# Kernel tuning notes

Hardware: AMD Instinct MI355X
Metric: run time of the kernel (lower is better)

The kernel has to match this reference:

```python
import jax, jax.numpy as jnp
import numpy as np

B, LI, LJ, D = 32, 512, 512, 512
NN_DIM = 256  # agg output dim = 2*NN_DIM = 512


def setup_inputs() -> dict:
    key = jax.random.key(0)
    k1, k2, k3 = jax.random.split(key, 3)
    i = jax.random.normal(k1, (B, LI, D), dtype=jnp.float32)
    j = jax.random.normal(k2, (B, LJ, D), dtype=jnp.float32)
    W_agg = jax.random.normal(k3, (D, 2 * NN_DIM), dtype=jnp.float32) * (1.0 / np.sqrt(D))
    b_agg = jnp.zeros((2 * NN_DIM,), dtype=jnp.float32)
    return {"i": i, "j": j, "W_agg": W_agg, "b_agg": b_agg}


def _agg(x, W, b):
    # shared aggregation net: Dense(2*nn_dim) + tanh, then mean-pool over time
    # x: [B, L, D] -> [B, 2*nn_dim]
    return jnp.mean(jnp.tanh(jnp.einsum('bld,dh->blh', x, W) + b), axis=1)


def reference(i, j, W_agg, b_agg):
    # cross-attention scores: [B, Li, Lj]
    weight = jnp.einsum('bik,bjk->bij', i, j)
    # row softmax (over Lj) -> weights to aggregate j per i-position
    weight_j = jax.nn.softmax(weight, axis=2)
    # column softmax (over Li) -> weights to aggregate i per j-position
    weight_i = jax.nn.softmax(weight, axis=1)
    weighted_i = jnp.einsum('bij,bid->bjd', weight_i, i)  # [B, Lj, D]
    weighted_j = jnp.einsum('bij,bjd->bid', weight_j, j)  # [B, Li, D]
    output_i = jnp.abs(i - weighted_j)  # [B, Li, D]
    output_j = jnp.abs(j - weighted_i)  # [B, Lj, D]
    oi = _agg(output_i, W_agg, b_agg)   # [B, 2*nn_dim]
    oj = _agg(output_j, W_agg, b_agg)   # [B, 2*nn_dim]
    # K.mean(K.stack([oi, oj], axis=1), axis=1)
    return 0.5 * (oi + oj)
```

## Files before the change

### kernel.cpp

```cpp
#include <hip/hip_runtime.h>
#include <math.h>

#define B_ 32
#define L_ 512
#define D_ 512
#define H_ 512

typedef unsigned short u16;
typedef _Float16 h16;
typedef h16 half8 __attribute__((ext_vector_type(8)));
typedef float f32x4 __attribute__((ext_vector_type(4)));

#define SW(r, c) ((c) ^ (((r) >> 1) & 3))

typedef __attribute__((address_space(1))) void gvoid;
typedef __attribute__((address_space(3))) void svoid;
__device__ __forceinline__ void async_cp16(const void* g, void* l) {
    __builtin_amdgcn_global_load_lds((gvoid*)g, (svoid*)l, 16, 0, 0);
}

__device__ __forceinline__ u16 f2h(float x) {
    h16 h = (h16)x;
    u16 r;
    __builtin_memcpy(&r, &h, 2);
    return r;
}
__device__ __forceinline__ float h2f(u16 u) {
    h16 h;
    __builtin_memcpy(&h, &u, 2);
    return (float)h;
}
__device__ __forceinline__ float fast_tanh(float x) {
    return 1.0f - 2.0f / (__expf(2.0f * x) + 1.0f);
}

__device__ __forceinline__ void xcd_decode16(int n, int& z, int& tile) {
    int xcd = n & 7, w = n >> 3;
    z = xcd + 8 * (w >> 4);
    tile = w & 15;
}

__global__ __launch_bounds__(256) void cvt_all(const float* __restrict__ I,
                                               const float* __restrict__ Jm,
                                               const float* __restrict__ W,
                                               u16* __restrict__ Ih, u16* __restrict__ IhT,
                                               u16* __restrict__ Jh, u16* __restrict__ JhT,
                                               u16* __restrict__ WT,
                                               float* __restrict__ out) {
    const int z = blockIdx.z;
    const float* src;
    u16* h;
    u16* hT;
    size_t base;
    if (z < 32) {
        src = I; h = Ih; hT = IhT; base = (size_t)z * 512 * 512;
    } else if (z < 64) {
        src = Jm; h = Jh; hT = JhT; base = (size_t)(z - 32) * 512 * 512;
    } else {
        src = W; h = nullptr; hT = WT; base = 0;
        out[(blockIdx.y * 8 + blockIdx.x) * 256 + threadIdx.x] = 0.0f;
    }
    const int r0 = blockIdx.y * 64, c0 = blockIdx.x * 64;
    __shared__ u16 t[64][66];
    const int tid = threadIdx.x;
    const int tr = tid >> 4, tc4 = (tid & 15) * 4;
#pragma unroll
    for (int rep = 0; rep < 4; ++rep) {
        int r = rep * 16 + tr;
        f32x4 v = *(const f32x4*)(src + base + (size_t)(r0 + r) * 512 + c0 + tc4);
        unsigned h0 = f2h(v[0]), h1 = f2h(v[1]), h2 = f2h(v[2]), h3 = f2h(v[3]);
        if (h)
            *(uint2*)(h + base + (size_t)(r0 + r) * 512 + c0 + tc4) =
                make_uint2(h0 | (h1 << 16), h2 | (h3 << 16));
        t[r][tc4] = (u16)h0; t[r][tc4 + 1] = (u16)h1;
        t[r][tc4 + 2] = (u16)h2; t[r][tc4 + 3] = (u16)h3;
    }
    __syncthreads();
#pragma unroll
    for (int rep = 0; rep < 4; ++rep) {
        int r = rep * 16 + tr;
        unsigned a = t[tc4][r], b = t[tc4 + 1][r], c = t[tc4 + 2][r], d = t[tc4 + 3][r];
        *(uint2*)(hT + base + (size_t)(c0 + r) * 512 + r0 + tc4) =
            make_uint2(a | (b << 16), c | (d << 16));
    }
}

__global__ __launch_bounds__(256, 2) void score_mfma(const u16* __restrict__ Ih,
                                                     const u16* __restrict__ Jh,
                                                     u16* __restrict__ P_un,
                                                     u16* __restrict__ P_unT,
                                                     float* __restrict__ rtmax,
                                                     float* __restrict__ rtsum,
                                                     float* __restrict__ ctmax,
                                                     float* __restrict__ ctsum) {
    int b, tile;
    xcd_decode16(blockIdx.x, b, tile);
    const int i0 = (tile >> 2) * 128, j0 = (tile & 3) * 128;
    __shared__ u16 Ah[128 * 32], Bh[128 * 32];
    const int tid = threadIdx.x;
    const int wave = tid >> 6, lane = tid & 63;
    const int wm = (wave >> 1) * 64, wn = (wave & 1) * 64;
    const int lr = lane & 15, q = lane >> 4;
    const size_t boff = (size_t)b * L_ * D_;
    const u16* Ibh = Ih + boff;
    const u16* Jbh = Jh + boff;

    f32x4 acc[4][4] = {};

    for (int k0 = 0; k0 < D_; k0 += 32) {
#pragma unroll
        for (int h = 0; h < 2; ++h) {
            int g = wave * 2 + h;
            int r = g * 16 + (lane >> 2);
            int cg = SW(r, lane & 3);
            async_cp16(Ibh + (size_t)(i0 + r) * D_ + k0 + cg * 8, (char*)Ah + g * 1024);
            async_cp16(Jbh + (size_t)(j0 + r) * D_ + k0 + cg * 8, (char*)Bh + g * 1024);
        }
        __syncthreads();
        half8 af[4], bf[4];
#pragma unroll
        for (int mi = 0; mi < 4; ++mi) {
            int r = wm + mi * 16 + lr;
            af[mi] = *(const half8*)&Ah[r * 32 + SW(r, q) * 8];
        }
#pragma unroll
        for (int ni = 0; ni < 4; ++ni) {
            int r = wn + ni * 16 + lr;
            bf[ni] = *(const half8*)&Bh[r * 32 + SW(r, q) * 8];
        }
#pragma unroll
        for (int mi = 0; mi < 4; ++mi)
#pragma unroll
            for (int ni = 0; ni < 4; ++ni)
                acc[mi][ni] = __builtin_amdgcn_mfma_f32_16x16x32_f16(af[mi], bf[ni], acc[mi][ni], 0, 0, 0);
        __syncthreads();
    }

    float rm[4][4];
#pragma unroll
    for (int mi = 0; mi < 4; ++mi)
#pragma unroll
        for (int r4 = 0; r4 < 4; ++r4) {
            float t = fmaxf(fmaxf(acc[mi][0][r4], acc[mi][1][r4]),
                            fmaxf(acc[mi][2][r4], acc[mi][3][r4]));
#pragma unroll
            for (int off = 1; off < 16; off <<= 1) t = fmaxf(t, __shfl_xor(t, off));
            rm[mi][r4] = t;
        }
    float cm[4];
#pragma unroll
    for (int ni = 0; ni < 4; ++ni) {
        float u = -1e30f;
#pragma unroll
        for (int mi = 0; mi < 4; ++mi)
#pragma unroll
            for (int r4 = 0; r4 < 4; ++r4) u = fmaxf(u, acc[mi][ni][r4]);
        u = fmaxf(u, __shfl_xor(u, 16));
        u = fmaxf(u, __shfl_xor(u, 32));
        cm[ni] = u;
    }

    u16* Pu_b = P_un + (size_t)b * L_ * L_;
    u16* PuT_b = P_unT + (size_t)b * L_ * L_;
    float rs[4][4] = {};
    float cs[4] = {};
#pragma unroll
    for (int mi = 0; mi < 4; ++mi)
#pragma unroll
        for (int ni = 0; ni < 4; ++ni) {
            int i_base = i0 + wm + mi * 16 + q * 4;
            int j = j0 + wn + ni * 16 + lr;
            unsigned pc[4];
#pragma unroll
            for (int r4 = 0; r4 < 4; ++r4) {
                float er = __expf(acc[mi][ni][r4] - rm[mi][r4]);
                rs[mi][r4] += er;
                Pu_b[(size_t)(i_base + r4) * L_ + j] = f2h(er);
                float ec = __expf(acc[mi][ni][r4] - cm[ni]);
                cs[ni] += ec;
                pc[r4] = f2h(ec);
            }
            *(uint2*)&PuT_b[(size_t)j * L_ + i_base] =
                make_uint2(pc[0] | (pc[1] << 16), pc[2] | (pc[3] << 16));
        }

    const int gr = (j0 + wn) >> 6;
    const int gc = (i0 + wm) >> 6;
#pragma unroll
    for (int mi = 0; mi < 4; ++mi)
#pragma unroll
        for (int r4 = 0; r4 < 4; ++r4) {
            float s = rs[mi][r4];
#pragma unroll
            for (int off = 1; off < 16; off <<= 1) s += __shfl_xor(s, off);
            if (lr == 0) {
                int i = i0 + wm + mi * 16 + q * 4 + r4;
                rtmax[((size_t)b * L_ + i) * 8 + gr] = rm[mi][r4];
                rtsum[((size_t)b * L_ + i) * 8 + gr] = s;
            }
        }
#pragma unroll
    for (int ni = 0; ni < 4; ++ni) {
        float s = cs[ni];
        s += __shfl_xor(s, 16);
        s += __shfl_xor(s, 32);
        if (q == 0) {
            int j = j0 + wn + ni * 16 + lr;
            ctmax[((size_t)b * L_ + j) * 8 + gc] = cm[ni];
            ctsum[((size_t)b * L_ + j) * 8 + gc] = s;
        }
    }
}

__global__ __launch_bounds__(256, 2) void absdiff_scaled(const u16* __restrict__ P_un,
                                                         const u16* __restrict__ P_unT,
                                                         const float* __restrict__ rtmax,
                                                         const float* __restrict__ rtsum,
                                                         const float* __restrict__ ctmax,
                                                         const float* __restrict__ ctsum,
                                                         const u16* __restrict__ JhT,
                                                         const u16* __restrict__ IhT,
                                                         const u16* __restrict__ Ih,
                                                         const u16* __restrict__ Jh,
                                                         u16* __restrict__ Xall) {
    int zz, tile;
    xcd_decode16(blockIdx.x, zz, tile);
    const int side = zz >> 5, b = zz & 31;
    const int a0 = (tile >> 2) * 128, d0 = (tile & 3) * 128;
    const u16* Pb = (side ? P_unT : P_un) + (size_t)b * L_ * L_;
    const float* tmax = (side ? ctmax : rtmax) + (size_t)b * L_ * 8;
    const float* tsum = (side ? ctsum : rtsum) + (size_t)b * L_ * 8;
    const u16* Vt = (side ? IhT : JhT) + (size_t)b * D_ * L_;
    const u16* Oh = (side ? Jh : Ih) + (size_t)b * L_ * D_;
    u16* Xb = Xall + (size_t)zz * L_ * D_;

    __shared__ u16 As[128 * 32], Bs[128 * 32];
    __shared__ float sc[8][128];
    const int tid = threadIdx.x;
    const int wave = tid >> 6, lane = tid & 63;
    const int wm = (wave >> 1) * 64, wn = (wave & 1) * 64;
    const int lr = lane & 15, q = lane >> 4;

    if (tid < 128) {
        const float* tm = tmax + (size_t)(a0 + tid) * 8;
        const float* ts = tsum + (size_t)(a0 + tid) * 8;
        f32x4 m0 = *(const f32x4*)tm, m1 = *(const f32x4*)(tm + 4);
        f32x4 s0 = *(const f32x4*)ts, s1 = *(const f32x4*)(ts + 4);
        float m = fmaxf(fmaxf(fmaxf(m0[0], m0[1]), fmaxf(m0[2], m0[3])),
                        fmaxf(fmaxf(m1[0], m1[1]), fmaxf(m1[2], m1[3])));
        float e0 = __expf(m0[0] - m), e1 = __expf(m0[1] - m);
        float e2 = __expf(m0[2] - m), e3 = __expf(m0[3] - m);
        float e4 = __expf(m1[0] - m), e5 = __expf(m1[1] - m);
        float e6 = __expf(m1[2] - m), e7 = __expf(m1[3] - m);
        float inv = 1.0f / (e0 * s0[0] + e1 * s0[1] + e2 * s0[2] + e3 * s0[3] +
                            e4 * s1[0] + e5 * s1[1] + e6 * s1[2] + e7 * s1[3]);
        sc[0][tid] = e0 * inv; sc[1][tid] = e1 * inv;
        sc[2][tid] = e2 * inv; sc[3][tid] = e3 * inv;
        sc[4][tid] = e4 * inv; sc[5][tid] = e5 * inv;
        sc[6][tid] = e6 * inv; sc[7][tid] = e7 * inv;
    }
    __syncthreads();

    f32x4 acc[4][4] = {};

    for (int k0 = 0; k0 < L_; k0 += 32) {
#pragma unroll
        for (int h = 0; h < 2; ++h) {
            int g = wave * 2 + h;
            int r = g * 16 + (lane >> 2);
            int cg = SW(r, lane & 3);
            async_cp16(Pb + (size_t)(a0 + r) * L_ + k0 + cg * 8, (char*)As + g * 1024);
            async_cp16(Vt + (size_t)(d0 + r) * L_ + k0 + cg * 8, (char*)Bs + g * 1024);
        }
        __syncthreads();
        const int gk = k0 >> 6;
        half8 af[4], bf[4];
#pragma unroll
        for (int mi = 0; mi < 4; ++mi) {
            int r = wm + mi * 16 + lr;
            h16 s = (h16)sc[gk][r];
            half8 s8 = {s, s, s, s, s, s, s, s};
            af[mi] = *(const half8*)&As[r * 32 + SW(r, q) * 8] * s8;
        }
#pragma unroll
        for (int ni = 0; ni < 4; ++ni) {
            int r = wn + ni * 16 + lr;
            bf[ni] = *(const half8*)&Bs[r * 32 + SW(r, q) * 8];
        }
#pragma unroll
        for (int mi = 0; mi < 4; ++mi)
#pragma unroll
            for (int ni = 0; ni < 4; ++ni)
                acc[mi][ni] = __builtin_amdgcn_mfma_f32_16x16x32_f16(af[mi], bf[ni], acc[mi][ni], 0, 0, 0);
        __syncthreads();
    }

#pragma unroll
    for (int mi = 0; mi < 4; ++mi)
#pragma unroll
        for (int ni = 0; ni < 4; ++ni) {
            int i = a0 + wm + mi * 16 + q * 4;
            int d = d0 + wn + ni * 16 + lr;
#pragma unroll
            for (int r4 = 0; r4 < 4; ++r4) {
                float x = fabsf(h2f(Oh[(size_t)(i + r4) * D_ + d]) - acc[mi][ni][r4]);
                Xb[(size_t)(i + r4) * D_ + d] = f2h(x);
            }
        }
}

__global__ __launch_bounds__(256, 2) void agg_mfma(const u16* __restrict__ Xall,
                                                   const u16* __restrict__ Wt,
                                                   const float* __restrict__ bias,
                                                   float* __restrict__ out) {
    int zz, tile;
    xcd_decode16(blockIdx.x, zz, tile);
    const int bb = zz & 31;
    const u16* Xb = Xall + (size_t)zz * L_ * D_;
    const int l0 = (tile >> 2) * 128, h0 = (tile & 3) * 128;
    __shared__ u16 As[128 * 32], Bs[128 * 32];
    const int tid = threadIdx.x;
    const int wave = tid >> 6, lane = tid & 63;
    const int wm = (wave >> 1) * 64, wn = (wave & 1) * 64;
    const int lr = lane & 15, q = lane >> 4;

    f32x4 acc[4][4] = {};

    for (int k0 = 0; k0 < D_; k0 += 32) {
#pragma unroll
        for (int h = 0; h < 2; ++h) {
            int g = wave * 2 + h;
            int r = g * 16 + (lane >> 2);
            int cg = SW(r, lane & 3);
            async_cp16(Xb + (size_t)(l0 + r) * D_ + k0 + cg * 8, (char*)As + g * 1024);
            async_cp16(Wt + (size_t)(h0 + r) * D_ + k0 + cg * 8, (char*)Bs + g * 1024);
        }
        __syncthreads();
        half8 af[4], bf[4];
#pragma unroll
        for (int mi = 0; mi < 4; ++mi) {
            int r = wm + mi * 16 + lr;
            af[mi] = *(const half8*)&As[r * 32 + SW(r, q) * 8];
        }
#pragma unroll
        for (int ni = 0; ni < 4; ++ni) {
            int r = wn + ni * 16 + lr;
            bf[ni] = *(const half8*)&Bs[r * 32 + SW(r, q) * 8];
        }
#pragma unroll
        for (int mi = 0; mi < 4; ++mi)
#pragma unroll
            for (int ni = 0; ni < 4; ++ni)
                acc[mi][ni] = __builtin_amdgcn_mfma_f32_16x16x32_f16(af[mi], bf[ni], acc[mi][ni], 0, 0, 0);
        __syncthreads();
    }

#pragma unroll
    for (int ni = 0; ni < 4; ++ni) {
        int hcol = h0 + wn + ni * 16 + lr;
        float bsv = bias[hcol];
        float ssum = 0.f;
#pragma unroll
        for (int mi = 0; mi < 4; ++mi)
#pragma unroll
            for (int r4 = 0; r4 < 4; ++r4)
                ssum += fast_tanh(acc[mi][ni][r4] + bsv);
        ssum += __shfl_xor(ssum, 16);
        ssum += __shfl_xor(ssum, 32);
        if (q == 0) atomicAdd(&out[bb * H_ + hcol], ssum * (0.5f / (float)L_));
    }
}

extern "C" void kernel_launch(void* const* d_in, const int* in_sizes, int n_in,
                              void* d_out, int out_size, void* d_ws, size_t ws_size,
                              hipStream_t stream) {
    const float* I = (const float*)d_in[0];
    const float* Jm = (const float*)d_in[1];
    const float* W = (const float*)d_in[2];
    const float* bias = (const float*)d_in[3];
    float* out = (float*)d_out;

    const size_t BLD = (size_t)B_ * L_ * D_;
    const size_t BLL = (size_t)B_ * L_ * L_;

    char* p = (char*)d_ws;
    auto give = [&](size_t bytes) {
        char* r = p;
        p += (bytes + 255) & ~(size_t)255;
        return r;
    };
    u16* Ih = (u16*)give(BLD * 2);
    u16* Jh = (u16*)give(BLD * 2);
    u16* IhT = (u16*)give(BLD * 2);
    u16* JhT = (u16*)give(BLD * 2);
    u16* WT = (u16*)give((size_t)D_ * H_ * 2);
    u16* P_un = (u16*)give(BLL * 2);
    u16* P_unT = (u16*)give(BLL * 2);
    float* rtmax = (float*)give((size_t)B_ * L_ * 8 * 4);
    float* rtsum = (float*)give((size_t)B_ * L_ * 8 * 4);
    float* ctmax = (float*)give((size_t)B_ * L_ * 8 * 4);
    float* ctsum = (float*)give((size_t)B_ * L_ * 8 * 4);
    u16* Xall = (u16*)give(2 * BLD * 2);

    cvt_all<<<dim3(8, 8, 65), 256, 0, stream>>>(I, Jm, W, Ih, IhT, Jh, JhT, WT, out);
    score_mfma<<<512, 256, 0, stream>>>(Ih, Jh, P_un, P_unT, rtmax, rtsum, ctmax, ctsum);
    absdiff_scaled<<<1024, 256, 0, stream>>>(P_un, P_unT, rtmax, rtsum, ctmax, ctsum,
                                             JhT, IhT, Ih, Jh, Xall);
    agg_mfma<<<1024, 256, 0, stream>>>(Xall, WT, bias, out);
}
```

Before: 190.3 us.

## Fuse absdiff and aggregation GEMMs into one kernel keeping X in LDS

Merges the weighted-sum/abs-diff kernel and the Dense+tanh+mean aggregation kernel into one kernel. Each block handles a 64-row slab over the full D, keeps the fp16 abs-diff tile in shared memory, then multiplies it by W directly. This removes the 32 MB Xall round trip through global memory and one launch. In exchange the grid drops to 512 blocks with 64-row tiles, so there is less reuse per MFMA tile. Shared memory per block grows to about 75 KB, which can lower occupancy.

```diff
diff --git a/kernel.cpp b/kernel.cpp
--- a/kernel.cpp
+++ b/kernel.cpp
@@ -38,6 +38,11 @@
     int xcd = n & 7, w = n >> 3;
     z = xcd + 8 * (w >> 4);
     tile = w & 15;
+}
+__device__ __forceinline__ void xcd_decode8(int n, int& z, int& tile) {
+    int xcd = n & 7, w = n >> 3;
+    z = xcd + 8 * (w >> 3);
+    tile = w & 7;
 }
 
 __global__ __launch_bounds__(256) void cvt_all(const float* __restrict__ I,
@@ -212,38 +217,41 @@
     }
 }
 
-__global__ __launch_bounds__(256, 2) void absdiff_scaled(const u16* __restrict__ P_un,
-                                                         const u16* __restrict__ P_unT,
-                                                         const float* __restrict__ rtmax,
-                                                         const float* __restrict__ rtsum,
-                                                         const float* __restrict__ ctmax,
-                                                         const float* __restrict__ ctsum,
-                                                         const u16* __restrict__ JhT,
-                                                         const u16* __restrict__ IhT,
-                                                         const u16* __restrict__ Ih,
-                                                         const u16* __restrict__ Jh,
-                                                         u16* __restrict__ Xall) {
-    int zz, tile;
-    xcd_decode16(blockIdx.x, zz, tile);
+__global__ __launch_bounds__(256, 2) void fused_tail(const u16* __restrict__ P_un,
+                                                     const u16* __restrict__ P_unT,
+                                                     const float* __restrict__ rtmax,
+                                                     const float* __restrict__ rtsum,
+                                                     const float* __restrict__ ctmax,
+                                                     const float* __restrict__ ctsum,
+                                                     const u16* __restrict__ JhT,
+                                                     const u16* __restrict__ IhT,
+                                                     const u16* __restrict__ Ih,
+                                                     const u16* __restrict__ Jh,
+                                                     const u16* __restrict__ Wt,
+                                                     const float* __restrict__ bias,
+                                                     float* __restrict__ out) {
+    int zz, ltile;
+    xcd_decode8(blockIdx.x, zz, ltile);
     const int side = zz >> 5, b = zz & 31;
-    const int a0 = (tile >> 2) * 128, d0 = (tile & 3) * 128;
+    const int l0 = ltile * 64;
     const u16* Pb = (side ? P_unT : P_un) + (size_t)b * L_ * L_;
     const float* tmax = (side ? ctmax : rtmax) + (size_t)b * L_ * 8;
     const float* tsum = (side ? ctsum : rtsum) + (size_t)b * L_ * 8;
     const u16* Vt = (side ? IhT : JhT) + (size_t)b * D_ * L_;
     const u16* Oh = (side ? Jh : Ih) + (size_t)b * L_ * D_;
-    u16* Xb = Xall + (size_t)zz * L_ * D_;
-
-    __shared__ u16 As[128 * 32], Bs[128 * 32];
-    __shared__ float sc[8][128];
+
+    __shared__ u16 Xs[64][520];
+    __shared__ u16 As[64 * 32];
+    __shared__ u16 Bs[128 * 32];
+    __shared__ float sc[8][64];
     const int tid = threadIdx.x;
     const int wave = tid >> 6, lane = tid & 63;
-    const int wm = (wave >> 1) * 64, wn = (wave & 1) * 64;
+    const int wm = (wave >> 1) * 32, wn = (wave & 1) * 64;
     const int lr = lane & 15, q = lane >> 4;
 
-    if (tid < 128) {
-        const float* tm = tmax + (size_t)(a0 + tid) * 8;
-        const float* ts = tsum + (size_t)(a0 + tid) * 8;
+    if (tid < 64) {
+        const float* tm = tmax + (size_t)(l0 + tid) * 8;
+        const float* ts = tsum + (size_t)(l0 + tid) * 8;
         f32x4 m0 = *(const f32x4*)tm, m1 = *(const f32x4*)(tm + 4);
         f32x4 s0 = *(const f32x4*)ts, s1 = *(const f32x4*)(ts + 4);
         float m = fmaxf(fmaxf(fmaxf(m0[0], m0[1]), fmaxf(m0[2], m0[3])),
@@ -261,113 +269,107 @@
     }
     __syncthreads();
 
-    f32x4 acc[4][4] = {};
-
-    for (int k0 = 0; k0 < L_; k0 += 32) {
-#pragma unroll
-        for (int h = 0; h < 2; ++h) {
-            int g = wave * 2 + h;
-            int r = g * 16 + (lane >> 2);
-            int cg = SW(r, lane & 3);
-            async_cp16(Pb + (size_t)(a0 + r) * L_ + k0 + cg * 8, (char*)As + g * 1024);
-            async_cp16(Vt + (size_t)(d0 + r) * L_ + k0 + cg * 8, (char*)Bs + g * 1024);
-        }
-        __syncthreads();
-        const int gk = k0 >> 6;
-        half8 af[4], bf[4];
-#pragma unroll
-        for (int mi = 0; mi < 4; ++mi) {
-            int r = wm + mi * 16 + lr;
-            h16 s = (h16)sc[gk][r];
-            half8 s8 = {s, s, s, s, s, s, s, s};
-            af[mi] = *(const half8*)&As[r * 32 + SW(r, q) * 8] * s8;
+#pragma unroll 1
+    for (int c = 0; c < 4; ++c) {
+        const int d0 = c * 128;
+        f32x4 acc[2][4] = {};
+        for (int k0 = 0; k0 < L_; k0 += 32) {
+            {
+                int r = wave * 16 + (lane >> 2);
+                int cg = SW(r, lane & 3);
+                async_cp16(Pb + (size_t)(l0 + r) * L_ + k0 + cg * 8, (char*)As + wave * 1024);
+            }
+#pragma unroll
+            for (int h = 0; h < 2; ++h) {
+                int g = wave * 2 + h;
+                int r = g * 16 + (lane >> 2);
+                int cg = SW(r, lane & 3);
+                async_cp16(Vt + (size_t)(d0 + r) * L_ + k0 + cg * 8, (char*)Bs + g * 1024);
+            }
+            __syncthreads();
+            const int gk = k0 >> 6;
+            half8 af[2], bf[4];
+#pragma unroll
+            for (int mi = 0; mi < 2; ++mi) {
+                int r = wm + mi * 16 + lr;
+                h16 s = (h16)sc[gk][r];
+                half8 s8 = {s, s, s, s, s, s, s, s};
+                af[mi] = *(const half8*)&As[r * 32 + SW(r, q) * 8] * s8;
+            }
+#pragma unroll
+            for (int ni = 0; ni < 4; ++ni) {
+                int r = wn + ni * 16 + lr;
+                bf[ni] = *(const half8*)&Bs[r * 32 + SW(r, q) * 8];
+            }
+#pragma unroll
+            for (int mi = 0; mi < 2; ++mi)
+#pragma unroll
+                for (int ni = 0; ni < 4; ++ni)
+                    acc[mi][ni] = __builtin_amdgcn_mfma_f32_16x16x32_f16(af[mi], bf[ni], acc[mi][ni], 0, 0, 0);
+            __syncthreads();
+        }
+#pragma unroll
+        for (int mi = 0; mi < 2; ++mi)
+#pragma unroll
+            for (int ni = 0; ni < 4; ++ni) {
+                int row = wm + mi * 16 + q * 4;
+                int col = wn + ni * 16 + lr;
+#pragma unroll
+                for (int r4 = 0; r4 < 4; ++r4) {
+                    float x = fabsf(h2f(Oh[(size_t)(l0 + row + r4) * D_ + d0 + col]) -
+                                    acc[mi][ni][r4]);
+                    Xs[row + r4][d0 + col] = f2h(x);
+                }
+            }
+    }
+    __syncthreads();
+
+    const int bb = b;
+#pragma unroll 1
+    for (int c = 0; c < 4; ++c) {
+        const int h0 = c * 128;
+        f32x4 acc[2][4] = {};
+        for (int k0 = 0; k0 < D_; k0 += 32) {
+#pragma unroll
+            for (int h = 0; h < 2; ++h) {
+                int g = wave * 2 + h;
+                int r = g * 16 + (lane >> 2);
+                int cg = SW(r, lane & 3);
+                async_cp16(Wt + (size_t)(h0 + r) * D_ + k0 + cg * 8, (char*)Bs + g * 1024);
+            }
+            __syncthreads();
+            half8 af[2], bf[4];
+#pragma unroll
+            for (int mi = 0; mi < 2; ++mi) {
+                int r = wm + mi * 16 + lr;
+                af[mi] = *(const half8*)&Xs[r][k0 + q * 8];
+            }
+#pragma unroll
+            for (int ni = 0; ni < 4; ++ni) {
+                int r = wn + ni * 16 + lr;
+                bf[ni] = *(const half8*)&Bs[r * 32 + SW(r, q) * 8];
+            }
+#pragma unroll
+            for (int mi = 0; mi < 2; ++mi)
+#pragma unroll
+                for (int ni = 0; ni < 4; ++ni)
+                    acc[mi][ni] = __builtin_amdgcn_mfma_f32_16x16x32_f16(af[mi], bf[ni], acc[mi][ni], 0, 0, 0);
+            __syncthreads();
         }
 #pragma unroll
         for (int ni = 0; ni < 4; ++ni) {
-            int r = wn + ni * 16 + lr;
-            bf[ni] = *(const half8*)&Bs[r * 32 + SW(r, q) * 8];
-        }
-#pragma unroll
-        for (int mi = 0; mi < 4; ++mi)
-#pragma unroll
-            for (int ni = 0; ni < 4; ++ni)
-                acc[mi][ni] = __builtin_amdgcn_mfma_f32_16x16x32_f16(af[mi], bf[ni], acc[mi][ni], 0, 0, 0);
-        __syncthreads();
-    }
-
-#pragma unroll
-    for (int mi = 0; mi < 4; ++mi)
-#pragma unroll
-        for (int ni = 0; ni < 4; ++ni) {
-            int i = a0 + wm + mi * 16 + q * 4;
-            int d = d0 + wn + ni * 16 + lr;
-#pragma unroll
-            for (int r4 = 0; r4 < 4; ++r4) {
-                float x = fabsf(h2f(Oh[(size_t)(i + r4) * D_ + d]) - acc[mi][ni][r4]);
-                Xb[(size_t)(i + r4) * D_ + d] = f2h(x);
-            }
-        }
-}
-
-__global__ __launch_bounds__(256, 2) void agg_mfma(const u16* __restrict__ Xall,
-                                                   const u16* __restrict__ Wt,
-                                                   const float* __restrict__ bias,
-                                                   float* __restrict__ out) {
-    int zz, tile;
-    xcd_decode16(blockIdx.x, zz, tile);
-    const int bb = zz & 31;
-    const u16* Xb = Xall + (size_t)zz * L_ * D_;
-    const int l0 = (tile >> 2) * 128, h0 = (tile & 3) * 128;
-    __shared__ u16 As[128 * 32], Bs[128 * 32];
-    const int tid = threadIdx.x;
-    const int wave = tid >> 6, lane = tid & 63;
-    const int wm = (wave >> 1) * 64, wn = (wave & 1) * 64;
-    const int lr = lane & 15, q = lane >> 4;
-
-    f32x4 acc[4][4] = {};
-
-    for (int k0 = 0; k0 < D_; k0 += 32) {
-#pragma unroll
-        for (int h = 0; h < 2; ++h) {
-            int g = wave * 2 + h;
-            int r = g * 16 + (lane >> 2);
-            int cg = SW(r, lane & 3);
-            async_cp16(Xb + (size_t)(l0 + r) * D_ + k0 + cg * 8, (char*)As + g * 1024);
-            async_cp16(Wt + (size_t)(h0 + r) * D_ + k0 + cg * 8, (char*)Bs + g * 1024);
-        }
-        __syncthreads();
-        half8 af[4], bf[4];
-#pragma unroll
-        for (int mi = 0; mi < 4; ++mi) {
-            int r = wm + mi * 16 + lr;
-            af[mi] = *(const half8*)&As[r * 32 + SW(r, q) * 8];
-        }
-#pragma unroll
-        for (int ni = 0; ni < 4; ++ni) {
-            int r = wn + ni * 16 + lr;
-            bf[ni] = *(const half8*)&Bs[r * 32 + SW(r, q) * 8];
-        }
-#pragma unroll
-        for (int mi = 0; mi < 4; ++mi)
-#pragma unroll
-            for (int ni = 0; ni < 4; ++ni)
-                acc[mi][ni] = __builtin_amdgcn_mfma_f32_16x16x32_f16(af[mi], bf[ni], acc[mi][ni], 0, 0, 0);
-        __syncthreads();
-    }
-
-#pragma unroll
-    for (int ni = 0; ni < 4; ++ni) {
-        int hcol = h0 + wn + ni * 16 + lr;
-        float bsv = bias[hcol];
-        float ssum = 0.f;
-#pragma unroll
-        for (int mi = 0; mi < 4; ++mi)
-#pragma unroll
-            for (int r4 = 0; r4 < 4; ++r4)
-                ssum += fast_tanh(acc[mi][ni][r4] + bsv);
-        ssum += __shfl_xor(ssum, 16);
-        ssum += __shfl_xor(ssum, 32);
-        if (q == 0) atomicAdd(&out[bb * H_ + hcol], ssum * (0.5f / (float)L_));
+            int hcol = h0 + wn + ni * 16 + lr;
+            float bsv = bias[hcol];
+            float ssum = 0.f;
+#pragma unroll
+            for (int mi = 0; mi < 2; ++mi)
+#pragma unroll
+                for (int r4 = 0; r4 < 4; ++r4)
+                    ssum += fast_tanh(acc[mi][ni][r4] + bsv);
+            ssum += __shfl_xor(ssum, 16);
+            ssum += __shfl_xor(ssum, 32);
+            if (q == 0) atomicAdd(&out[bb * H_ + hcol], ssum * (0.5f / (float)L_));
+        }
     }
 }
 
@@ -400,11 +402,9 @@
     float* rtsum = (float*)give((size_t)B_ * L_ * 8 * 4);
     float* ctmax = (float*)give((size_t)B_ * L_ * 8 * 4);
     float* ctsum = (float*)give((size_t)B_ * L_ * 8 * 4);
-    u16* Xall = (u16*)give(2 * BLD * 2);
 
     cvt_all<<<dim3(8, 8, 65), 256, 0, stream>>>(I, Jm, W, Ih, IhT, Jh, JhT, WT, out);
     score_mfma<<<512, 256, 0, stream>>>(Ih, Jh, P_un, P_unT, rtmax, rtsum, ctmax, ctsum);
-    absdiff_scaled<<<1024, 256, 0, stream>>>(P_un, P_unT, rtmax, rtsum, ctmax, ctsum,
-                                             JhT, IhT, Ih, Jh, Xall);
-    agg_mfma<<<1024, 256, 0, stream>>>(Xall, WT, bias, out);
-}
+    fused_tail<<<512, 256, 0, stream>>>(P_un, P_unT, rtmax, rtsum, ctmax, ctsum,
+                                        JhT, IhT, Ih, Jh, WT, bias, out);
+}
```

New measurement: 219.8 us. 15.5% more time.
